# Optimization experiments

Hardware: AMD Instinct MI355X
Metric: run time of the kernel (lower is better)

The kernel has to match this reference:

```python
import jax, jax.numpy as jnp
import numpy as np

NUM_HEADS = 16
THETA = 10000.0
B, S, D = 2, 2048, 1024
D_K = D // NUM_HEADS


def setup_inputs() -> dict:
    key = jax.random.key(0)
    ks = jax.random.split(key, 5)
    s = 0.02
    return {
        "x": jax.random.normal(ks[0], (B, S, D), dtype=jnp.float32),
        "W_q": jax.random.normal(ks[1], (D, D), dtype=jnp.float32) * s,
        "W_k": jax.random.normal(ks[2], (D, D), dtype=jnp.float32) * s,
        "W_v": jax.random.normal(ks[3], (D, D), dtype=jnp.float32) * s,
        "W_o": jax.random.normal(ks[4], (D, D), dtype=jnp.float32) * s,
        "token_positions": jnp.arange(S, dtype=jnp.int32),
    }


def _rope(x, token_positions):
    # x: [..., seq, d_k]; equivalent to the block-diagonal 2x2 rotation matmul
    d2 = x.shape[-1] // 2
    inv_freq = THETA ** (-(2.0 * jnp.arange(d2, dtype=x.dtype)) / x.shape[-1])  # [d2]
    ang = token_positions.astype(x.dtype)[:, None] * inv_freq[None, :]  # [seq, d2]
    cos, sin = jnp.cos(ang), jnp.sin(ang)
    xp = x.reshape(x.shape[:-1] + (d2, 2))
    xe, xo = xp[..., 0], xp[..., 1]
    oe = cos * xe - sin * xo
    oo = sin * xe + cos * xo
    return jnp.stack([oe, oo], axis=-1).reshape(x.shape)


def reference(x, W_q, W_k, W_v, W_o, token_positions):
    seq = x.shape[-2]
    # QKV projections (weights stored as [out, in])
    Q = jnp.einsum('bsd,ed->bse', x, W_q)
    K = jnp.einsum('bsd,ed->bse', x, W_k)
    V = jnp.einsum('bsd,ed->bse', x, W_v)
    def split_heads(t):
        return t.reshape(t.shape[:-1] + (NUM_HEADS, D_K)).swapaxes(-3, -2)  # [b,h,s,dk]
    Q, K, V = split_heads(Q), split_heads(K), split_heads(V)
    Q = _rope(Q, token_positions)
    K = _rope(K, token_positions)
    scale = 1.0 / np.sqrt(D_K)
    scores = jnp.einsum('bhqd,bhkd->bhqk', Q, K) * scale
    causal = jnp.tril(jnp.ones((seq, seq), dtype=bool))
    scores = jnp.where(causal, scores, -jnp.inf)
    probs = jax.nn.softmax(scores, axis=-1)
    out = jnp.einsum('bhqk,bhkd->bhqd', probs, V)
    out = out.swapaxes(-3, -2).reshape(x.shape[:-1] + (D,))
    return jnp.einsum('bse,de->bsd', out, W_o)
```

## Files before the change

kernel.cpp:

```cpp
#include <hip/hip_runtime.h>
#include <hip/hip_bf16.h>
#include <math.h>

#define H_    16
#define DK_   64
#define Dm    1024
#define Bb    2
#define Ss    2048
#define Mrows 4096
#define QSCALE 0.1803368801f

typedef short s16x8 __attribute__((ext_vector_type(8)));
typedef float f32x4 __attribute__((ext_vector_type(4)));
typedef unsigned short u16;
typedef unsigned int u32;

__device__ __forceinline__ u16 f2b(float f) {
  __hip_bfloat16 h = __float2bfloat16(f);
  return *reinterpret_cast<u16*>(&h);
}
__device__ __forceinline__ float b2f(u16 u) {
  __hip_bfloat16 h;
  *reinterpret_cast<u16*>(&h) = u;
  return __bfloat162float(h);
}
__device__ __forceinline__ u32 pkbf(float hi, float lo) {
  return __builtin_amdgcn_perm(__float_as_uint(hi), __float_as_uint(lo), 0x07060302u);
}

#define GLDS(g, l)                                                             \
  __builtin_amdgcn_global_load_lds(                                            \
      (const __attribute__((address_space(1))) unsigned int*)(g),              \
      (__attribute__((address_space(3))) unsigned int*)(l), 16, 0, 0)

__device__ __forceinline__ int SW64(int row, int col) {
  return row * 64 + ((((col >> 3) ^ (row & 7) ^ (row >> 3)) & 7) << 3) + (col & 7);
}

__global__ __launch_bounds__(256) void k_castall(
    const float* __restrict__ x,  const float* __restrict__ Wq,
    const float* __restrict__ Wk, const float* __restrict__ Wv,
    const float* __restrict__ Wo,
    u16* __restrict__ xb,  u16* __restrict__ wqb, u16* __restrict__ wkb,
    u16* __restrict__ wvb, u16* __restrict__ wob,
    const int* __restrict__ pos, float2* __restrict__ tab) {
  if (blockIdx.x >= 8192) {
    int t = (blockIdx.x - 8192) * 256 + threadIdx.x;
    int s = t >> 5, i = t & 31;
    float p = (float)pos[s];
    float ang = p * __builtin_amdgcn_exp2f(-(float)i * 0.4152448120604907f);
    tab[t] = make_float2(cosf(ang), sinf(ang));
    return;
  }
  int i = blockIdx.x * 256 + threadIdx.x;
  const float* s;
  u16* d;
  int off;
  if (i < 1048576) { s = x; d = xb; off = i; }
  else {
    int j = i - 1048576;
    int w = j >> 18;
    off = j & 262143;
    s = (w == 0) ? Wq : (w == 1) ? Wk : (w == 2) ? Wv : Wo;
    d = (w == 0) ? wqb : (w == 1) ? wkb : (w == 2) ? wvb : wob;
  }
  float4 v = reinterpret_cast<const float4*>(s)[off];
  ushort4 o;
  o.x = f2b(v.x); o.y = f2b(v.y); o.z = f2b(v.z); o.w = f2b(v.w);
  reinterpret_cast<ushort4*>(d)[off] = o;
}

__global__ __launch_bounds__(256) void k_ropeK(u16* __restrict__ K,
                                               const float2* __restrict__ tab) {
  int t = blockIdx.x * 256 + threadIdx.x;
  int row = t >> 7;
  int c0 = (t & 127) << 3;
  int i0 = (c0 & 63) >> 1;
  const float2* tb = &tab[(row & (Ss - 1)) * 32 + i0];
  float2 cs[4];
#pragma unroll
  for (int j = 0; j < 4; ++j) cs[j] = tb[j];
  size_t off = (size_t)row * Dm + c0;
  s16x8 k = *reinterpret_cast<const s16x8*>(&K[off]);
  s16x8 ko;
#pragma unroll
  for (int j = 0; j < 4; ++j) {
    float ke = b2f((u16)k[2 * j]), kd = b2f((u16)k[2 * j + 1]);
    ko[2 * j]     = (short)f2b(cs[j].x * ke - cs[j].y * kd);
    ko[2 * j + 1] = (short)f2b(cs[j].y * ke + cs[j].x * kd);
  }
  *reinterpret_cast<s16x8*>(&K[off]) = ko;
}

template <int BN, bool QKV>
__global__ __launch_bounds__(256) void k_gemm(
    const u16* __restrict__ A, const u16* __restrict__ B,
    u16* __restrict__ OQ, u16* __restrict__ OK2, u16* __restrict__ OVT,
    float* __restrict__ OF, int K) {
  constexpr int NFR = BN / 32;
  __shared__ __align__(16) u16 lsA[3][128 * 32];
  __shared__ __align__(16) u16 lsB[3][BN * 32];
  const int tid = threadIdx.x, lane = tid & 63, wave = tid >> 6;
  const int quad = lane >> 4, l16 = lane & 15;
  const int wrow = wave >> 1, wcol = wave & 1;
  const int n0 = blockIdx.x * BN, m0 = blockIdx.y * 128;
  f32x4 acc[4][NFR] = {};

  auto stage = [&](int k0, int bi) {
#pragma unroll
    for (int c = 0; c < 2; ++c) {
      int f = (wave * 2 + c) * 64 + lane;
      int row = f >> 2;
      int gs = (f & 3) ^ ((row >> 1) & 3);
      GLDS(A + (size_t)(m0 + row) * K + k0 + gs * 8, &lsA[bi][(wave * 2 + c) * 512]);
    }
#pragma unroll
    for (int c = 0; c < NFR / 2; ++c) {
      int f = (wave * (NFR / 2) + c) * 64 + lane;
      int row = f >> 2;
      int gs = (f & 3) ^ ((row >> 1) & 3);
      GLDS(B + (size_t)(n0 + row) * K + k0 + gs * 8, &lsB[bi][(wave * (NFR / 2) + c) * 512]);
    }
  };

  stage(0, 0);
  stage(32, 1);
  int bi = 0, stg = 2;
  for (int k0 = 0; k0 < K; k0 += 32) {
    if (k0 + 32 < K) {
      if constexpr (NFR == 4) asm volatile("s_waitcnt vmcnt(4)" ::: "memory");
      else                    asm volatile("s_waitcnt vmcnt(3)" ::: "memory");
    } else {
      asm volatile("s_waitcnt vmcnt(0)" ::: "memory");
    }
    __builtin_amdgcn_sched_barrier(0);
    __builtin_amdgcn_s_barrier();
    if (k0 + 64 < K) stage(k0 + 64, stg);
    s16x8 af[4], bfr[NFR];
#pragma unroll
    for (int i = 0; i < 4; ++i) {
      int row = wrow * 64 + i * 16 + l16;
      af[i] = *reinterpret_cast<const s16x8*>(
          &lsA[bi][row * 32 + ((quad ^ ((row >> 1) & 3)) << 3)]);
    }
#pragma unroll
    for (int i = 0; i < NFR; ++i) {
      int row = wcol * (BN / 2) + i * 16 + l16;
      bfr[i] = *reinterpret_cast<const s16x8*>(
          &lsB[bi][row * 32 + ((quad ^ ((row >> 1) & 3)) << 3)]);
    }
#pragma unroll
    for (int mi = 0; mi < 4; ++mi)
#pragma unroll
      for (int ni = 0; ni < NFR; ++ni)
        acc[mi][ni] = __builtin_amdgcn_mfma_f32_16x16x32_bf16(af[mi], bfr[ni], acc[mi][ni], 0, 0, 0);
    stg = bi;
    bi = (bi == 2) ? 0 : bi + 1;
  }

  if (QKV) {
    const int which = n0 >> 10;
    const int nbase = (n0 & 1023) + wcol * (BN / 2);
    if (which == 2) {
#pragma unroll
      for (int mi = 0; mi < 4; ++mi)
#pragma unroll
        for (int ni = 0; ni < NFR; ++ni) {
          int row0 = m0 + wrow * 64 + mi * 16 + quad * 4;
          int col  = nbase + ni * 16 + l16;
          int bb = row0 >> 11, s0 = row0 & (Ss - 1);
          ushort4 pk;
          pk.x = f2b(acc[mi][ni][0]); pk.y = f2b(acc[mi][ni][1]);
          pk.z = f2b(acc[mi][ni][2]); pk.w = f2b(acc[mi][ni][3]);
          *reinterpret_cast<ushort4*>(&OVT[((size_t)bb * Dm + col) * Ss + s0]) = pk;
        }
    } else {
      u16* Op = which ? OK2 : OQ;
#pragma unroll
      for (int mi = 0; mi < 4; ++mi)
#pragma unroll
        for (int ni = 0; ni < NFR; ++ni)
#pragma unroll
          for (int r = 0; r < 4; ++r) {
            int row = m0 + wrow * 64 + mi * 16 + quad * 4 + r;
            int col = nbase + ni * 16 + l16;
            Op[(size_t)row * Dm + col] = f2b(acc[mi][ni][r]);
          }
    }
  } else {
#pragma unroll
    for (int mi = 0; mi < 4; ++mi)
#pragma unroll
      for (int ni = 0; ni < NFR; ++ni)
#pragma unroll
        for (int r = 0; r < 4; ++r) {
          int row = m0 + wrow * 64 + mi * 16 + quad * 4 + r;
          int col = n0 + wcol * (BN / 2) + ni * 16 + l16;
          OF[(size_t)row * Dm + col] = acc[mi][ni][r];
        }
  }
}

__global__ __launch_bounds__(256) void k_flash(const u16* __restrict__ Q,
                                               const u16* __restrict__ K,
                                               const u16* __restrict__ VT,
                                               u16* __restrict__ O,
                                               const float2* __restrict__ tab) {
  __shared__ __align__(16) u16 lsK[4][64 * 64];
  __shared__ __align__(16) u16 lsVT[4][64 * 64];
  __shared__ __align__(16) u16 lsP[4][32 * 64];
  const int tid = threadIdx.x, lane = tid & 63, wave = tid >> 6;
  const int quad = lane >> 4, l16 = lane & 15;
  const int bid = blockIdx.x;
  const int bh = bid & 31;
  const int h = bh & (H_ - 1), b = bh >> 4;
  const int g = bid >> 5, a = g & 7, bsel = g >> 3;
  const int qt = bsel ? (15 - a) : a;
  const int q0 = qt * 128;
  const int qbase = q0 + wave * 32;
  const int ktmax_w = (qbase + 31) >> 6;
  const int xorv = (l16 * 2) & 0xE;

  s16x8 qf[2][2];
#pragma unroll
  for (int s = 0; s < 2; ++s) {
    const int qpos = qbase + s * 16 + l16;
    const size_t qoff = (size_t)(b * Ss + qpos) * Dm + h * 64;
    s16x8 r0 = *reinterpret_cast<const s16x8*>(&Q[qoff + quad * 8]);
    s16x8 r1 = *reinterpret_cast<const s16x8*>(&Q[qoff + 32 + quad * 8]);
    const float2* tb = &tab[(qpos & (Ss - 1)) * 32];
#pragma unroll
    for (int kc = 0; kc < 2; ++kc) {
      s16x8 raw = kc ? r1 : r0;
#pragma unroll
      for (int p = 0; p < 4; ++p) {
        float2 cs = tb[kc * 16 + quad * 4 + p];
        float e = b2f((u16)raw[2 * p]), o = b2f((u16)raw[2 * p + 1]);
        qf[s][kc][2 * p]     = (short)f2b((cs.x * e - cs.y * o) * QSCALE);
        qf[s][kc][2 * p + 1] = (short)f2b((cs.y * e + cs.x * o) * QSCALE);
      }
    }
  }
  s16x8 ones;
#pragma unroll
  for (int j = 0; j < 8; ++j) ones[j] = (short)0x3F80;

  f32x4 ot[2][4] = {};
  f32x4 lAcc[2] = {};

  auto stage1 = [&](int kt) {
    const int slot = kt & 3;
    const size_t kbase  = (size_t)(b * Ss + kt * 64) * Dm + h * 64;
    const size_t vtbase = ((size_t)b * Dm + h * 64) * Ss + kt * 64;
#pragma unroll
    for (int c = 0; c < 2; ++c) {
      int sl = (wave * 2 + c) * 64 + lane;
      int row = sl >> 3;
      int gg = ((sl & 7) ^ (row & 7) ^ (row >> 3)) & 7;
      GLDS(K  + kbase  + (size_t)row * Dm + gg * 8, &lsK[slot][(wave * 2 + c) * 512]);
      GLDS(VT + vtbase + (size_t)row * Ss + gg * 8, &lsVT[slot][(wave * 2 + c) * 512]);
    }
  };

  const int ktend = 2 * qt + 2;
  stage1(0);
  stage1(1);
  for (int kt = 0; kt < ktend; ++kt) {
    if (kt + 1 < ktend) asm volatile("s_waitcnt vmcnt(4)" ::: "memory");
    else                asm volatile("s_waitcnt vmcnt(0)" ::: "memory");
    __builtin_amdgcn_sched_barrier(0);
    __builtin_amdgcn_s_barrier();
    __builtin_amdgcn_sched_barrier(0);
    if (kt + 2 < ktend) stage1(kt + 2);
    if (kt > ktmax_w) continue;
    const int slot = kt & 3;

    f32x4 st[2][4] = {};
    __builtin_amdgcn_s_setprio(1);
#pragma unroll
    for (int kc = 0; kc < 2; ++kc)
#pragma unroll
      for (int ni = 0; ni < 4; ++ni) {
        s16x8 kf = *reinterpret_cast<const s16x8*>(
            &lsK[slot][SW64(ni * 16 + l16, kc * 32 + quad * 8)]);
        st[0][ni] = __builtin_amdgcn_mfma_f32_16x16x32_bf16(kf, qf[0][kc], st[0][ni], 0, 0, 0);
        st[1][ni] = __builtin_amdgcn_mfma_f32_16x16x32_bf16(kf, qf[1][kc], st[1][ni], 0, 0, 0);
      }
    __builtin_amdgcn_s_setprio(0);

    if (kt == ktmax_w) {
#pragma unroll
      for (int s = 0; s < 2; ++s) {
        int gq = qbase + s * 16 + l16;
#pragma unroll
        for (int ni = 0; ni < 4; ++ni)
#pragma unroll
          for (int r = 0; r < 4; ++r)
            if (kt * 64 + ni * 16 + quad * 4 + r > gq) st[s][ni][r] = -INFINITY;
      }
    }
#pragma unroll
    for (int s = 0; s < 2; ++s)
#pragma unroll
      for (int ni = 0; ni < 4; ++ni) {
        float e0 = __builtin_amdgcn_exp2f(st[s][ni][0]);
        float e1 = __builtin_amdgcn_exp2f(st[s][ni][1]);
        float e2 = __builtin_amdgcn_exp2f(st[s][ni][2]);
        float e3 = __builtin_amdgcn_exp2f(st[s][ni][3]);
        uint2 pk;
        pk.x = pkbf(e1, e0);
        pk.y = pkbf(e3, e2);
        *reinterpret_cast<uint2*>(
            &lsP[wave][(s * 16 + l16) * 64 + (((ni * 4 + quad) ^ xorv) << 2)]) = pk;
      }
#pragma unroll
    for (int kc = 0; kc < 2; ++kc) {
      s16x8 pf0 = *reinterpret_cast<const s16x8*>(
          &lsP[wave][l16 * 64 + (((kc * 8 + quad * 2) ^ xorv) << 2)]);
      s16x8 pf1 = *reinterpret_cast<const s16x8*>(
          &lsP[wave][(16 + l16) * 64 + (((kc * 8 + quad * 2) ^ xorv) << 2)]);
      __builtin_amdgcn_s_setprio(1);
      lAcc[0] = __builtin_amdgcn_mfma_f32_16x16x32_bf16(ones, pf0, lAcc[0], 0, 0, 0);
      lAcc[1] = __builtin_amdgcn_mfma_f32_16x16x32_bf16(ones, pf1, lAcc[1], 0, 0, 0);
#pragma unroll
      for (int ni = 0; ni < 4; ++ni) {
        s16x8 vf = *reinterpret_cast<const s16x8*>(
            &lsVT[slot][SW64(ni * 16 + l16, kc * 32 + quad * 8)]);
        ot[0][ni] = __builtin_amdgcn_mfma_f32_16x16x32_bf16(vf, pf0, ot[0][ni], 0, 0, 0);
        ot[1][ni] = __builtin_amdgcn_mfma_f32_16x16x32_bf16(vf, pf1, ot[1][ni], 0, 0, 0);
      }
      __builtin_amdgcn_s_setprio(0);
    }
  }

#pragma unroll
  for (int s = 0; s < 2; ++s) {
    float inv = 1.0f / lAcc[s][0];
    const size_t obase = (size_t)(b * Ss + qbase + s * 16 + l16) * Dm + h * 64;
#pragma unroll
    for (int ni = 0; ni < 4; ++ni) {
      ushort4 pk;
      pk.x = f2b(ot[s][ni][0] * inv); pk.y = f2b(ot[s][ni][1] * inv);
      pk.z = f2b(ot[s][ni][2] * inv); pk.w = f2b(ot[s][ni][3] * inv);
      *reinterpret_cast<ushort4*>(&O[obase + ni * 16 + quad * 4]) = pk;
    }
  }
}

extern "C" void kernel_launch(void* const* d_in, const int* in_sizes, int n_in,
                              void* d_out, int out_size, void* d_ws, size_t ws_size,
                              hipStream_t stream) {
  const float* x  = (const float*)d_in[0];
  const float* Wq = (const float*)d_in[1];
  const float* Wk = (const float*)d_in[2];
  const float* Wv = (const float*)d_in[3];
  const float* Wo = (const float*)d_in[4];
  const int* pos  = (const int*)d_in[5];
  float* out = (float*)d_out;

  char* w = (char*)d_ws;
  u16* xb  = (u16*)w; w += (size_t)Mrows * Dm * 2;
  u16* wqb = (u16*)w; w += (size_t)Dm * Dm * 2;
  u16* wkb = (u16*)w; w += (size_t)Dm * Dm * 2;
  u16* wvb = (u16*)w; w += (size_t)Dm * Dm * 2;
  u16* wob = (u16*)w; w += (size_t)Dm * Dm * 2;
  u16* Qb  = (u16*)w; w += (size_t)Mrows * Dm * 2;
  u16* Kb  = (u16*)w; w += (size_t)Mrows * Dm * 2;
  u16* VTb = (u16*)w; w += (size_t)Mrows * Dm * 2;
  u16* Ab  = (u16*)w; w += (size_t)Mrows * Dm * 2;
  float2* tabf = (float2*)w; w += (size_t)Ss * 32 * sizeof(float2);

  k_castall<<<8448, 256, 0, stream>>>(x, Wq, Wk, Wv, Wo, xb, wqb, wkb, wvb, wob,
                                      pos, tabf);
  k_gemm<128, true><<<dim3(24, 32), 256, 0, stream>>>(xb, wqb, Qb, Kb, VTb, nullptr, Dm);
  k_ropeK<<<Mrows * Dm / 8 / 256, 256, 0, stream>>>(Kb, tabf);
  k_flash<<<dim3(512), 256, 0, stream>>>(Qb, Kb, VTb, Ab, tabf);
  k_gemm<64, false><<<dim3(16, 32), 256, 0, stream>>>(Ab, wob, nullptr, nullptr, nullptr, out, Dm);
}
```

Before: 190.7 us.

## Shrink flash attention query tile to 64 rows and double the grid

The flash kernel now gives each block 64 query rows (16 per wave) instead of 128, and launches 1024 blocks instead of 512. The K/V LDS ring drops from four slots with two tiles in flight to two slots with a simple one-ahead prefetch under __syncthreads. The explicit vmcnt waits and s_setprio hints are removed. The aim is more parallelism, a smaller LDS footprint for higher occupancy, and less causal-tail imbalance. The cost is that each K/V tile is reused by half as many query rows, which doubles K/V traffic, and the prefetch depth is shallower.

```diff
diff --git a/kernel.cpp b/kernel.cpp
--- a/kernel.cpp
+++ b/kernel.cpp
@@ -206,29 +206,26 @@
                                                const u16* __restrict__ VT,
                                                u16* __restrict__ O,
                                                const float2* __restrict__ tab) {
-  __shared__ __align__(16) u16 lsK[4][64 * 64];
-  __shared__ __align__(16) u16 lsVT[4][64 * 64];
-  __shared__ __align__(16) u16 lsP[4][32 * 64];
+  __shared__ __align__(16) u16 lsK[2][64 * 64];
+  __shared__ __align__(16) u16 lsVT[2][64 * 64];
+  __shared__ __align__(16) u16 lsP[4][16 * 64];
   const int tid = threadIdx.x, lane = tid & 63, wave = tid >> 6;
   const int quad = lane >> 4, l16 = lane & 15;
   const int bid = blockIdx.x;
   const int bh = bid & 31;
   const int h = bh & (H_ - 1), b = bh >> 4;
-  const int g = bid >> 5, a = g & 7, bsel = g >> 3;
-  const int qt = bsel ? (15 - a) : a;
-  const int q0 = qt * 128;
-  const int qbase = q0 + wave * 32;
-  const int ktmax_w = (qbase + 31) >> 6;
+  const int g = bid >> 5, a = g & 15, bsel = g >> 4;
+  const int qt = bsel ? (31 - a) : a;
+  const int qbase = qt * 64 + wave * 16;
   const int xorv = (l16 * 2) & 0xE;
 
-  s16x8 qf[2][2];
-#pragma unroll
-  for (int s = 0; s < 2; ++s) {
-    const int qpos = qbase + s * 16 + l16;
+  s16x8 qf[2];
+  {
+    const int qpos = qbase + l16;
     const size_t qoff = (size_t)(b * Ss + qpos) * Dm + h * 64;
     s16x8 r0 = *reinterpret_cast<const s16x8*>(&Q[qoff + quad * 8]);
     s16x8 r1 = *reinterpret_cast<const s16x8*>(&Q[qoff + 32 + quad * 8]);
-    const float2* tb = &tab[(qpos & (Ss - 1)) * 32];
+    const float2* tb = &tab[qpos * 32];
 #pragma unroll
     for (int kc = 0; kc < 2; ++kc) {
       s16x8 raw = kc ? r1 : r0;
@@ -236,8 +233,8 @@
       for (int p = 0; p < 4; ++p) {
         float2 cs = tb[kc * 16 + quad * 4 + p];
         float e = b2f((u16)raw[2 * p]), o = b2f((u16)raw[2 * p + 1]);
-        qf[s][kc][2 * p]     = (short)f2b((cs.x * e - cs.y * o) * QSCALE);
-        qf[s][kc][2 * p + 1] = (short)f2b((cs.y * e + cs.x * o) * QSCALE);
+        qf[kc][2 * p]     = (short)f2b((cs.x * e - cs.y * o) * QSCALE);
+        qf[kc][2 * p + 1] = (short)f2b((cs.y * e + cs.x * o) * QSCALE);
       }
     }
   }
@@ -245,11 +242,11 @@
 #pragma unroll
   for (int j = 0; j < 8; ++j) ones[j] = (short)0x3F80;
 
-  f32x4 ot[2][4] = {};
-  f32x4 lAcc[2] = {};
+  f32x4 ot[4] = {};
+  f32x4 lAcc = {};
 
   auto stage1 = [&](int kt) {
-    const int slot = kt & 3;
+    const int slot = kt & 1;
     const size_t kbase  = (size_t)(b * Ss + kt * 64) * Dm + h * 64;
     const size_t vtbase = ((size_t)b * Dm + h * 64) * Ss + kt * 64;
 #pragma unroll
@@ -262,86 +259,65 @@
     }
   };
 
-  const int ktend = 2 * qt + 2;
+  const int ktend = qt + 1;
   stage1(0);
-  stage1(1);
   for (int kt = 0; kt < ktend; ++kt) {
-    if (kt + 1 < ktend) asm volatile("s_waitcnt vmcnt(4)" ::: "memory");
-    else                asm volatile("s_waitcnt vmcnt(0)" ::: "memory");
-    __builtin_amdgcn_sched_barrier(0);
-    __builtin_amdgcn_s_barrier();
-    __builtin_amdgcn_sched_barrier(0);
-    if (kt + 2 < ktend) stage1(kt + 2);
-    if (kt > ktmax_w) continue;
-    const int slot = kt & 3;
-
-    f32x4 st[2][4] = {};
-    __builtin_amdgcn_s_setprio(1);
+    __syncthreads();
+    if (kt + 1 < ktend) stage1(kt + 1);
+    const int slot = kt & 1;
+
+    f32x4 st[4] = {};
 #pragma unroll
     for (int kc = 0; kc < 2; ++kc)
 #pragma unroll
       for (int ni = 0; ni < 4; ++ni) {
         s16x8 kf = *reinterpret_cast<const s16x8*>(
             &lsK[slot][SW64(ni * 16 + l16, kc * 32 + quad * 8)]);
-        st[0][ni] = __builtin_amdgcn_mfma_f32_16x16x32_bf16(kf, qf[0][kc], st[0][ni], 0, 0, 0);
-        st[1][ni] = __builtin_amdgcn_mfma_f32_16x16x32_bf16(kf, qf[1][kc], st[1][ni], 0, 0, 0);
+        st[ni] = __builtin_amdgcn_mfma_f32_16x16x32_bf16(kf, qf[kc], st[ni], 0, 0, 0);
       }
-    __builtin_amdgcn_s_setprio(0);
-
-    if (kt == ktmax_w) {
-#pragma unroll
-      for (int s = 0; s < 2; ++s) {
-        int gq = qbase + s * 16 + l16;
-#pragma unroll
-        for (int ni = 0; ni < 4; ++ni)
-#pragma unroll
-          for (int r = 0; r < 4; ++r)
-            if (kt * 64 + ni * 16 + quad * 4 + r > gq) st[s][ni][r] = -INFINITY;
-      }
-    }
-#pragma unroll
-    for (int s = 0; s < 2; ++s)
-#pragma unroll
-      for (int ni = 0; ni < 4; ++ni) {
-        float e0 = __builtin_amdgcn_exp2f(st[s][ni][0]);
-        float e1 = __builtin_amdgcn_exp2f(st[s][ni][1]);
-        float e2 = __builtin_amdgcn_exp2f(st[s][ni][2]);
-        float e3 = __builtin_amdgcn_exp2f(st[s][ni][3]);
-        uint2 pk;
-        pk.x = pkbf(e1, e0);
-        pk.y = pkbf(e3, e2);
-        *reinterpret_cast<uint2*>(
-            &lsP[wave][(s * 16 + l16) * 64 + (((ni * 4 + quad) ^ xorv) << 2)]) = pk;
-      }
+
+    if (kt == qt) {
+      int gq = qbase + l16;
+#pragma unroll
+      for (int ni = 0; ni < 4; ++ni)
+#pragma unroll
+        for (int r = 0; r < 4; ++r)
+          if (kt * 64 + ni * 16 + quad * 4 + r > gq) st[ni][r] = -INFINITY;
+    }
+#pragma unroll
+    for (int ni = 0; ni < 4; ++ni) {
+      float e0 = __builtin_amdgcn_exp2f(st[ni][0]);
+      float e1 = __builtin_amdgcn_exp2f(st[ni][1]);
+      float e2 = __builtin_amdgcn_exp2f(st[ni][2]);
+      float e3 = __builtin_amdgcn_exp2f(st[ni][3]);
+      uint2 pk;
+      pk.x = pkbf(e1, e0);
+      pk.y = pkbf(e3, e2);
+      *reinterpret_cast<uint2*>(
+          &lsP[wave][l16 * 64 + (((ni * 4 + quad) ^ xorv) << 2)]) = pk;
+    }
 #pragma unroll
     for (int kc = 0; kc < 2; ++kc) {
-      s16x8 pf0 = *reinterpret_cast<const s16x8*>(
+      s16x8 pf = *reinterpret_cast<const s16x8*>(
           &lsP[wave][l16 * 64 + (((kc * 8 + quad * 2) ^ xorv) << 2)]);
-      s16x8 pf1 = *reinterpret_cast<const s16x8*>(
-          &lsP[wave][(16 + l16) * 64 + (((kc * 8 + quad * 2) ^ xorv) << 2)]);
-      __builtin_amdgcn_s_setprio(1);
-      lAcc[0] = __builtin_amdgcn_mfma_f32_16x16x32_bf16(ones, pf0, lAcc[0], 0, 0, 0);
-      lAcc[1] = __builtin_amdgcn_mfma_f32_16x16x32_bf16(ones, pf1, lAcc[1], 0, 0, 0);
+      lAcc = __builtin_amdgcn_mfma_f32_16x16x32_bf16(ones, pf, lAcc, 0, 0, 0);
 #pragma unroll
       for (int ni = 0; ni < 4; ++ni) {
         s16x8 vf = *reinterpret_cast<const s16x8*>(
             &lsVT[slot][SW64(ni * 16 + l16, kc * 32 + quad * 8)]);
-        ot[0][ni] = __builtin_amdgcn_mfma_f32_16x16x32_bf16(vf, pf0, ot[0][ni], 0, 0, 0);
-        ot[1][ni] = __builtin_amdgcn_mfma_f32_16x16x32_bf16(vf, pf1, ot[1][ni], 0, 0, 0);
+        ot[ni] = __builtin_amdgcn_mfma_f32_16x16x32_bf16(vf, pf, ot[ni], 0, 0, 0);
       }
-      __builtin_amdgcn_s_setprio(0);
-    }
-  }
-
-#pragma unroll
-  for (int s = 0; s < 2; ++s) {
-    float inv = 1.0f / lAcc[s][0];
-    const size_t obase = (size_t)(b * Ss + qbase + s * 16 + l16) * Dm + h * 64;
+    }
+  }
+
+  {
+    float inv = 1.0f / lAcc[0];
+    const size_t obase = (size_t)(b * Ss + qbase + l16) * Dm + h * 64;
 #pragma unroll
     for (int ni = 0; ni < 4; ++ni) {
       ushort4 pk;
-      pk.x = f2b(ot[s][ni][0] * inv); pk.y = f2b(ot[s][ni][1] * inv);
-      pk.z = f2b(ot[s][ni][2] * inv); pk.w = f2b(ot[s][ni][3] * inv);
+      pk.x = f2b(ot[ni][0] * inv); pk.y = f2b(ot[ni][1] * inv);
+      pk.z = f2b(ot[ni][2] * inv); pk.w = f2b(ot[ni][3] * inv);
       *reinterpret_cast<ushort4*>(&O[obase + ni * 16 + quad * 4]) = pk;
     }
   }
@@ -374,6 +350,6 @@
                                       pos, tabf);
   k_gemm<128, true><<<dim3(24, 32), 256, 0, stream>>>(xb, wqb, Qb, Kb, VTb, nullptr, Dm);
   k_ropeK<<<Mrows * Dm / 8 / 256, 256, 0, stream>>>(Kb, tabf);
-  k_flash<<<dim3(512), 256, 0, stream>>>(Qb, Kb, VTb, Ab, tabf);
+  k_flash<<<dim3(1024), 256, 0, stream>>>(Qb, Kb, VTb, Ab, tabf);
   k_gemm<64, false><<<dim3(16, 32), 256, 0, stream>>>(Ab, wob, nullptr, nullptr, nullptr, out, Dm);
 }
```

New measurement: 186.0 us. 1.03x faster.
